# Kernel tuning notes

Hardware: AMD Instinct MI355X
Metric: run time of the kernel (lower is better)

The kernel has to match this reference:

```python
import jax, jax.numpy as jnp
import numpy as np

B_SZ, L, D_MODEL = 2, 1024, 1024
EXPAND, D_STATE, D_CONV = 2, 16, 4
D_INNER = D_MODEL * EXPAND
DT_RANK = max(D_MODEL // 16, 1)


def setup_inputs() -> dict:
    key = jax.random.key(0)
    ks = jax.random.split(key, 9)
    s = 0.02
    x = jax.random.normal(ks[0], (B_SZ, L, D_MODEL), jnp.float32)
    W_in = jax.random.normal(ks[1], (2 * D_INNER, D_MODEL), jnp.float32) * s
    conv_w = jax.random.normal(ks[2], (D_INNER, D_CONV), jnp.float32) * 0.1
    conv_b = jax.random.normal(ks[3], (D_INNER,), jnp.float32) * 0.01
    W_x = jax.random.normal(ks[4], (DT_RANK + 2 * D_STATE, D_INNER), jnp.float32) * s
    W_dt = jax.random.normal(ks[5], (D_INNER, DT_RANK), jnp.float32) * s
    b_dt = jax.random.normal(ks[6], (D_INNER,), jnp.float32) * 0.01
    A_log = jnp.log(jnp.broadcast_to(jnp.arange(1, D_STATE + 1, dtype=jnp.float32), (D_INNER, D_STATE)))
    D_param = jnp.ones((D_INNER,), jnp.float32)
    W_out = jax.random.normal(ks[7], (D_MODEL, D_INNER), jnp.float32) * s
    return {"x": x, "W_in": W_in, "conv_w": conv_w, "conv_b": conv_b,
            "W_x": W_x, "W_dt": W_dt, "b_dt": b_dt, "A_log": A_log,
            "D_param": D_param, "W_out": W_out}


def _mamba_fwd(x, W_in, conv_w, conv_b, W_x, W_dt, b_dt, A_log, D_param, W_out):
    # in-proj and gate split
    xz = jnp.einsum("bld,ed->ble", x, W_in)            # (B, L, 2*d_inner)
    x_ssm, z = jnp.split(xz, 2, axis=-1)
    # causal depthwise 1D conv (left pad d_conv-1 == torch pad-both + [:L])
    xc = x_ssm.transpose(0, 2, 1)                        # (B, d_inner, L)
    xc = jax.lax.conv_general_dilated(
        xc, conv_w[:, None, :], window_strides=(1,),
        padding=[(D_CONV - 1, 0)], feature_group_count=D_INNER,
        dimension_numbers=("NCH", "OIH", "NCH"))
    xc = xc + conv_b[None, :, None]
    x_ssm = jax.nn.silu(xc.transpose(0, 2, 1))           # (B, L, d_inner)
    # input-dependent dt, B, C
    dbc = jnp.einsum("bld,ed->ble", x_ssm, W_x)
    dt, B_sel, C_sel = jnp.split(dbc, [DT_RANK, DT_RANK + D_STATE], axis=-1)
    delta = jax.nn.softplus(jnp.einsum("blr,dr->bld", dt, W_dt) + b_dt)
    A = -jnp.exp(A_log)                                  # (d_inner, d_state)
    # discretization
    deltaA = jnp.exp(delta[..., None] * A)               # (B, L, d_inner, d_state)
    dBu = delta[..., None] * B_sel[:, :, None, :] * x_ssm[..., None]
    # linear recurrence h_t = deltaA_t * h_{t-1} + dBu_t via associative scan
    def comb(e1, e2):
        a1, b1 = e1
        a2, b2 = e2
        return (a1 * a2, a2 * b1 + b2)
    _, h = jax.lax.associative_scan(comb, (deltaA, dBu), axis=1)
    y = jnp.sum(h * C_sel[:, :, None, :], axis=-1)       # (B, L, d_inner)
    y = y + x_ssm * D_param
    y = y * jax.nn.silu(z)
    return jnp.einsum("ble,de->bld", y, W_out)


def reference(x, W_in, conv_w, conv_b, W_x, W_dt, b_dt, A_log, D_param, W_out):
    return _mamba_fwd(x, W_in, conv_w, conv_b, W_x, W_dt, b_dt, A_log, D_param, W_out)
```

## Files before the change

### kernel.cpp

```cpp
#include <hip/hip_runtime.h>
#include <hip/hip_bf16.h>

#define B_SZ   2
#define SEQ    1024
#define DMODEL 1024
#define DINNER 2048
#define DSTATE 16
#define DCONV  4
#define DTRANK 64
#define BLROWS (B_SZ*SEQ)
#define NCHUNK 32
#define TCHUNK (SEQ/NCHUNK)
#define NSLICE 16

using floatx4 = __attribute__((ext_vector_type(4))) float;
using short8  = __attribute__((ext_vector_type(8))) short;
using us8     = __attribute__((ext_vector_type(8))) unsigned short;
using us4     = __attribute__((ext_vector_type(4))) unsigned short;

__device__ __forceinline__ float softplus_f(float x) {
    return fmaxf(x, 0.f) + log1pf(__expf(-fabsf(x)));
}
__device__ __forceinline__ float silu_f(float x) {
    return x / (1.f + __expf(-x));
}
__device__ __forceinline__ short bfs(float x) {
    union { __hip_bfloat16 h; short s; } u;
    u.h = __float2bfloat16(x);
    return u.s;
}
__device__ __forceinline__ float b2f(unsigned short s) {
    union { float f; unsigned u; } x;
    x.u = ((unsigned)s) << 16;
    return x.f;
}
__device__ __forceinline__ void gld16(const void* g, void* l) {
    __builtin_amdgcn_global_load_lds((const __attribute__((address_space(1))) void*)g,
                                     (__attribute__((address_space(3))) void*)l,
                                     16, 0, 0);
}
__device__ __forceinline__ void cast8(const float* src, unsigned short* dst, int i) {
    const float* p = src + (size_t)i*8;
    float4 a = *(const float4*)p, b = *(const float4*)(p+4);
    us8 o;
    o[0]=(unsigned short)bfs(a.x); o[1]=(unsigned short)bfs(a.y);
    o[2]=(unsigned short)bfs(a.z); o[3]=(unsigned short)bfs(a.w);
    o[4]=(unsigned short)bfs(b.x); o[5]=(unsigned short)bfs(b.y);
    o[6]=(unsigned short)bfs(b.z); o[7]=(unsigned short)bfs(b.w);
    *(us8*)(dst + (size_t)i*8) = o;
}

#define G0 (BLROWS*DMODEL/8)
#define G1 (2*DINNER*DMODEL/8)
#define G2 (96*DINNER/8)
#define G3 (DINNER*DTRANK/8)
#define G4 (DMODEL*DINNER/8)
#define GTOT (G0+G1+G2+G3+G4)
__global__ __launch_bounds__(256)
void init_kernel(const float* __restrict__ x, const float* __restrict__ W_in,
                 const float* __restrict__ W_x, const float* __restrict__ W_dt,
                 const float* __restrict__ W_out,
                 unsigned short* xH, unsigned short* WinH, unsigned short* WxH,
                 unsigned short* WdtH, unsigned short* WoutH)
{
    int i = blockIdx.x*256 + threadIdx.x;
    if (i < G0) { cast8(x, xH, i); return; }            i -= G0;
    if (i < G1) { cast8(W_in, WinH, i); return; }       i -= G1;
    if (i < G2) { cast8(W_x, WxH, i); return; }         i -= G2;
    if (i < G3) { cast8(W_dt, WdtH, i); return; }       i -= G3;
    if (i < G4) { cast8(W_out, WoutH, i); }
}

template<int TN, int EPI, bool NGUARD>
__global__ __launch_bounds__(256)
void gemm_tn(const __hip_bfloat16* __restrict__ Ag, const __hip_bfloat16* __restrict__ Bg,
             int M, int N, int K, int kslice,
             float* __restrict__ outF,
             __hip_bfloat16* __restrict__ outH,
             __hip_bfloat16* __restrict__ outH2,
             const float* __restrict__ bias)
{
    constexpr int EB  = TN/64;
    constexpr int FNW = TN/32;
    __shared__ short As[2][128*32];
    __shared__ short Bs[2][TN*32];

    const int tid  = threadIdx.x;
    const int lane = tid & 63, wave = tid >> 6;
    const int bm0  = blockIdx.x * 128;
    const int bn0  = blockIdx.y * TN;
    const int kbeg = blockIdx.z * kslice;
    const int kend = kbeg + kslice;
    const int wrow = (wave >> 1) * 64, wcol = (wave & 1) * (TN/2);
    const int lrow = lane & 15, quad = lane >> 4;

    const int srow = wave*16 + (lane >> 2);
    const int scol = (lane & 3) * 8;

    const __hip_bfloat16* ga0 = Ag + (size_t)(bm0 + srow)*K      + scol;
    const __hip_bfloat16* ga1 = Ag + (size_t)(bm0 + srow + 64)*K + scol;
    const __hip_bfloat16* gb0 = Bg + (size_t)(bn0 + srow)*K      + scol;
    const __hip_bfloat16* gb1 = (EB > 1) ? Bg + (size_t)(bn0 + srow + 64)*K + scol : nullptr;
    const bool b0ok = !NGUARD || (bn0 + wave*16) < N;
    const bool b1ok = (EB > 1) && (!NGUARD || (bn0 + wave*16 + 64) < N);

    auto stage = [&](int c, int k0) {
        gld16(ga0 + k0, &As[c][(wave*16)*32]);
        gld16(ga1 + k0, &As[c][(wave*16 + 64)*32]);
        if (b0ok) gld16(gb0 + k0, &Bs[c][(wave*16)*32]);
        if (EB > 1 && b1ok) gld16(gb1 + k0, &Bs[c][(wave*16 + 64)*32]);
    };

    floatx4 acc[4][FNW] = {};

    stage(0, kbeg);
    __syncthreads();
    int cur = 0;
    for (int k0 = kbeg; k0 < kend; k0 += 32) {
        if (k0 + 32 < kend) stage(cur ^ 1, k0 + 32);
        short8 af[4], bf[FNW];
        #pragma unroll
        for (int i = 0; i < 4; i++)
            af[i] = *(const short8*)&As[cur][(wrow + i*16 + lrow)*32 + quad*8];
        #pragma unroll
        for (int j = 0; j < FNW; j++)
            bf[j] = *(const short8*)&Bs[cur][(wcol + j*16 + lrow)*32 + quad*8];
        #pragma unroll
        for (int i = 0; i < 4; i++)
            #pragma unroll
            for (int j = 0; j < FNW; j++)
                acc[i][j] = __builtin_amdgcn_mfma_f32_16x16x32_bf16(af[i], bf[j], acc[i][j], 0, 0, 0);
        __syncthreads();
        cur ^= 1;
    }

    const int rq = quad * 4;
    #pragma unroll
    for (int i = 0; i < 4; i++) {
        #pragma unroll
        for (int j = 0; j < FNW; j++) {
            int col = bn0 + wcol + j*16 + lrow;
            if (NGUARD && col >= N) continue;
            if constexpr (EPI == 8) {
                int row0 = bm0 + wrow + i*16 + rq;
                int bb = row0 >> 10, ll = row0 & (SEQ-1);
                us4 pk;
                #pragma unroll
                for (int r = 0; r < 4; r++)
                    pk[r] = (unsigned short)bfs(softplus_f(acc[i][j][r] + bias[col]));
                *(us4*)((unsigned short*)outH + ((size_t)bb*DINNER + col)*SEQ + ll) = pk;
            } else {
                #pragma unroll
                for (int r = 0; r < 4; r++) {
                    int row = bm0 + wrow + i*16 + rq + r;
                    float v = acc[i][j][r];
                    if constexpr (EPI == 5) {
                        if (col < DINNER)
                            outH[(size_t)row*DINNER + col] = __float2bfloat16(v);
                        else
                            outH2[(size_t)row*DINNER + (col - DINNER)] = __float2bfloat16(v);
                    } else if constexpr (EPI == 9) {
                        outF[(size_t)blockIdx.z*M*N + (size_t)row*N + col] = v;
                    }
                }
            }
        }
    }
}

__global__ __launch_bounds__(192)
void dbc_reduce_kernel(const float* __restrict__ part, float* __restrict__ dbc,
                       __hip_bfloat16* __restrict__ dtH)
{
    const int tid = threadIdx.x;
    const int r2  = (tid >= 96) ? 1 : 0;
    const int col = tid - 96*r2;
    const int row = blockIdx.x*2 + r2;
    const size_t idx = (size_t)row*96 + col;
    float s = 0.f;
    #pragma unroll
    for (int z = 0; z < NSLICE; z++)
        s += part[(size_t)z*(BLROWS*96) + idx];
    dbc[idx] = s;
    if (col < DTRANK)
        dtH[(size_t)row*DTRANK + col] = __float2bfloat16(s);
}

__global__ __launch_bounds__(256)
void conv_transpose_kernel(const unsigned short* __restrict__ xbufN,
                           const float* __restrict__ cw,
                           const float* __restrict__ cb,
                           unsigned short* __restrict__ xsN,
                           unsigned short* __restrict__ xsT)
{
    __shared__ unsigned short t[67*68];
    __shared__ unsigned short t2[64*68];
    const int tid = threadIdx.x;
    const int l0 = blockIdx.x * 64, d0 = blockIdx.y * 64, b = blockIdx.z;

    const int lc4 = (tid & 15) * 4;
    for (int r = tid >> 4; r < 67; r += 16) {
        int lg = l0 - 3 + r;
        us4 v = {0,0,0,0};
        if (lg >= 0)
            v = *(const us4*)&xbufN[((size_t)(b*SEQ + lg))*DINNER + d0 + lc4];
        *(us4*)&t[r*68 + lc4] = v;
    }
    __syncthreads();

    const int dd = tid & 63;
    float4 w4 = *(const float4*)&cw[(d0 + dd)*4];
    float  bb = cb[d0 + dd];
    #pragma unroll 4
    for (int rr = tid >> 6; rr < 64; rr += 4) {
        float acc = bb;
        acc += w4.x * b2f(t[(rr+0)*68 + dd]);
        acc += w4.y * b2f(t[(rr+1)*68 + dd]);
        acc += w4.z * b2f(t[(rr+2)*68 + dd]);
        acc += w4.w * b2f(t[(rr+3)*68 + dd]);
        unsigned short h = (unsigned short)bfs(silu_f(acc));
        t2[rr*68 + dd] = h;
        xsN[((size_t)(b*SEQ + l0 + rr))*DINNER + d0 + dd] = h;
    }
    __syncthreads();

    const int dr = tid >> 4, lc = tid & 15;
    #pragma unroll
    for (int i = 0; i < 4; i++) {
        int dT = dr + i*16;
        us4 w;
        #pragma unroll
        for (int j = 0; j < 4; j++)
            w[j] = t2[(lc*4 + j)*68 + dT];
        *(us4*)&xsT[((size_t)b*DINNER + d0 + dT)*SEQ + l0 + lc*4] = w;
    }
}

__global__ __launch_bounds__(256)
void scan_pass1(const unsigned short* __restrict__ deT,
                const unsigned short* __restrict__ xsT,
                const float* __restrict__ dbc,
                const float* __restrict__ A_log,
                float* __restrict__ Bc, float* __restrict__ sde)
{
    __shared__ float bs[TCHUNK*16];
    const int tid  = threadIdx.x;
    const int q    = tid & 3, dsub = tid >> 2;
    const int blk  = blockIdx.x;
    const int dg   = blk & 31;
    const int c    = (blk >> 5) & (NCHUNK-1);
    const int b    = blk >> 10;
    const int d    = dg*64 + dsub;

    size_t b96 = (size_t)b*SEQ*96;
    if (tid < TCHUNK*4) {
        int r = tid >> 2, f = (tid & 3) * 4;
        *(float4*)&bs[r*16 + f] =
            *(const float4*)&dbc[b96 + (size_t)(c*TCHUNK + r)*96 + DTRANK + f];
    }

    float An[4];
    *(float4*)An = *(const float4*)&A_log[d*DSTATE + 4*q];
    #pragma unroll
    for (int j = 0; j < 4; j++) An[j] = -__expf(An[j]);

    size_t rowT = ((size_t)b*DINNER + d)*SEQ;
    __syncthreads();

    float h[4] = {0.f,0.f,0.f,0.f};
    float s = 0.f;
    for (int t8 = 0; t8 < TCHUNK/8; ++t8) {
        int l0 = c*TCHUNK + t8*8;
        us8 de8 = *(const us8*)&deT[rowT + l0];
        us8 u8  = *(const us8*)&xsT[rowT + l0];
        #pragma unroll
        for (int j2 = 0; j2 < 8; j2++) {
            int lr = t8*8 + j2;
            float Bn[4];
            *(float4*)Bn = *(const float4*)&bs[lr*16 + 4*q];
            float de = b2f(de8[j2]);
            float du = de * b2f(u8[j2]);
            #pragma unroll
            for (int j = 0; j < 4; j++)
                h[j] = __expf(de*An[j])*h[j] + du*Bn[j];
            s += de;
        }
    }
    size_t ci = (size_t)(b*NCHUNK + c)*DINNER + d;
    *(float4*)&Bc[ci*16 + 4*q] = *(float4*)h;
    if (q == 0) sde[ci] = s;
}

__global__ __launch_bounds__(256)
void scan_pass2(float* __restrict__ Bc, const float* __restrict__ sde,
                const float* __restrict__ A_log)
{
    const int tid = threadIdx.x;
    const int n   = tid & 15, dl = tid >> 4;
    const int blk = blockIdx.x;
    const int dg  = blk & 127, b = blk >> 7;
    const int d   = dg*16 + dl;
    const float An = -__expf(A_log[d*DSTATE + n]);

    float H = 0.f;
    for (int c = 0; c < NCHUNK; ++c) {
        size_t ci = (size_t)(b*NCHUNK + c)*DINNER + d;
        float bc = Bc[ci*16 + n];
        Bc[ci*16 + n] = H;
        H = __expf(An*sde[ci])*H + bc;
    }
}

__global__ __launch_bounds__(256)
void scan_pass3(const unsigned short* __restrict__ deT,
                const unsigned short* __restrict__ xsT,
                const float* __restrict__ dbc,
                const float* __restrict__ A_log,
                const float* __restrict__ Dp,
                const float* __restrict__ Hinit,
                const unsigned short* __restrict__ zN,
                __hip_bfloat16* __restrict__ yN)
{
    __shared__ float bcs[TCHUNK*32];
    const int tid  = threadIdx.x;
    const int q    = tid & 3, dsub = tid >> 2;
    const int blk  = blockIdx.x;
    const int dg   = blk & 31;
    const int c    = (blk >> 5) & (NCHUNK-1);
    const int b    = blk >> 10;
    const int d    = dg*64 + dsub;

    size_t b96 = (size_t)b*SEQ*96;
    {
        int r = tid >> 3, f = (tid & 7) * 4;
        *(float4*)&bcs[r*32 + f] =
            *(const float4*)&dbc[b96 + (size_t)(c*TCHUNK + r)*96 + DTRANK + f];
    }

    float An[4];
    *(float4*)An = *(const float4*)&A_log[d*DSTATE + 4*q];
    #pragma unroll
    for (int j = 0; j < 4; j++) An[j] = -__expf(An[j]);
    const float Dd = Dp[d];

    size_t rowT  = ((size_t)b*DINNER + d)*SEQ;
    size_t baseN = (size_t)b*SEQ*DINNER + d;

    float h[4];
    *(float4*)h = *(const float4*)&Hinit[((size_t)(b*NCHUNK + c)*DINNER + d)*16 + 4*q];
    __syncthreads();

    for (int t8 = 0; t8 < TCHUNK/8; ++t8) {
        int l0 = c*TCHUNK + t8*8;
        us8 de8 = *(const us8*)&deT[rowT + l0];
        us8 u8  = *(const us8*)&xsT[rowT + l0];
        #pragma unroll
        for (int j2 = 0; j2 < 8; j2++) {
            int l  = l0 + j2;
            int lr = t8*8 + j2;
            float Bn[4], Cn[4];
            *(float4*)Bn = *(const float4*)&bcs[lr*32 + 4*q];
            *(float4*)Cn = *(const float4*)&bcs[lr*32 + 16 + 4*q];
            float de = b2f(de8[j2]);
            float u  = b2f(u8[j2]);
            float du = de * u;
            float cc = 0.f;
            #pragma unroll
            for (int j = 0; j < 4; j++) {
                h[j] = __expf(de*An[j])*h[j] + du*Bn[j];
                cc += h[j]*Cn[j];
            }
            cc += __shfl_xor(cc, 1);
            cc += __shfl_xor(cc, 2);
            if (q == 0) {
                float zv = silu_f(b2f(zN[baseN + (size_t)l*DINNER]));
                yN[baseN + (size_t)l*DINNER] = __float2bfloat16((cc + u*Dd) * zv);
            }
        }
    }
}

__global__ __launch_bounds__(256)
void zero_out_kernel(float* out, int n) {
    int i = blockIdx.x * 256 + threadIdx.x;
    if (i < n) out[i] = 0.f;
}

extern "C" void kernel_launch(void* const* d_in, const int* in_sizes, int n_in,
                              void* d_out, int out_size, void* d_ws, size_t ws_size,
                              hipStream_t stream) {
    const float* x      = (const float*)d_in[0];
    const float* W_in   = (const float*)d_in[1];
    const float* conv_w = (const float*)d_in[2];
    const float* conv_b = (const float*)d_in[3];
    const float* W_x    = (const float*)d_in[4];
    const float* W_dt   = (const float*)d_in[5];
    const float* b_dt   = (const float*)d_in[6];
    const float* A_log  = (const float*)d_in[7];
    const float* D_par  = (const float*)d_in[8];
    const float* W_out  = (const float*)d_in[9];

    size_t szBig = (size_t)BLROWS * DINNER * 2;
    size_t szBc  = (size_t)B_SZ * NCHUNK * DINNER * DSTATE * 4;
    size_t need  = 5*szBig
                 + (size_t)BLROWS*96*4
                 + (size_t)NSLICE*BLROWS*96*4
                 + (size_t)BLROWS*DTRANK*2
                 + szBc + (size_t)B_SZ*NCHUNK*DINNER*4
                 + (size_t)BLROWS*DMODEL*2
                 + (size_t)2*DINNER*DMODEL*2
                 + (size_t)128*DINNER*2
                 + (size_t)DINNER*DTRANK*2
                 + (size_t)DMODEL*DINNER*2;

    if (ws_size < need) {
        zero_out_kernel<<<(out_size + 255)/256, 256, 0, stream>>>((float*)d_out, out_size);
        return;
    }

    char* w = (char*)d_ws;
    __hip_bfloat16* xbufN = (__hip_bfloat16*)w;  w += szBig;
    __hip_bfloat16* zbufN = (__hip_bfloat16*)w;  w += szBig;
    __hip_bfloat16* xsN   = (__hip_bfloat16*)w;  w += szBig;
    __hip_bfloat16* xsT   = (__hip_bfloat16*)w;  w += szBig;
    __hip_bfloat16* deT   = (__hip_bfloat16*)w;  w += szBig;
    float*          dbc   = (float*)w;           w += (size_t)BLROWS * 96 * 4;
    float*          dbcP  = (float*)w;           w += (size_t)NSLICE * BLROWS * 96 * 4;
    __hip_bfloat16* dtH   = (__hip_bfloat16*)w;  w += (size_t)BLROWS * DTRANK * 2;
    float*          Bc    = (float*)w;           w += szBc;
    float*          sde   = (float*)w;           w += (size_t)B_SZ * NCHUNK * DINNER * 4;
    __hip_bfloat16* xH    = (__hip_bfloat16*)w;  w += (size_t)BLROWS*DMODEL*2;
    __hip_bfloat16* WinH  = (__hip_bfloat16*)w;  w += (size_t)2*DINNER*DMODEL*2;
    __hip_bfloat16* WxH   = (__hip_bfloat16*)w;  w += (size_t)128*DINNER*2;
    __hip_bfloat16* WdtH  = (__hip_bfloat16*)w;  w += (size_t)DINNER*DTRANK*2;
    __hip_bfloat16* WoutH = (__hip_bfloat16*)w;  w += (size_t)DMODEL*DINNER*2;
    __hip_bfloat16* yN    = xsN;

    init_kernel<<<GTOT/256, 256, 0, stream>>>(x, W_in, W_x, W_dt, W_out,
        (unsigned short*)xH, (unsigned short*)WinH, (unsigned short*)WxH,
        (unsigned short*)WdtH, (unsigned short*)WoutH);

    gemm_tn<128,5,false><<<dim3(BLROWS/128, (2*DINNER)/128, 1), 256, 0, stream>>>(
        xH, WinH, BLROWS, 2*DINNER, DMODEL, DMODEL, nullptr, xbufN, zbufN, nullptr);

    conv_transpose_kernel<<<dim3(SEQ/64, DINNER/64, B_SZ), 256, 0, stream>>>(
        (const unsigned short*)xbufN, conv_w, conv_b,
        (unsigned short*)xsN, (unsigned short*)xsT);

    gemm_tn<64,9,true><<<dim3(BLROWS/128, 2, NSLICE), 256, 0, stream>>>(
        xsN, WxH, BLROWS, 96, DINNER, DINNER/NSLICE, dbcP, nullptr, nullptr, nullptr);
    dbc_reduce_kernel<<<BLROWS/2, 192, 0, stream>>>(dbcP, dbc, dtH);

    gemm_tn<64,8,false><<<dim3(BLROWS/128, DINNER/64, 1), 256, 0, stream>>>(
        dtH, WdtH, BLROWS, DINNER, DTRANK, DTRANK, nullptr, deT, nullptr, b_dt);

    scan_pass1<<<B_SZ*NCHUNK*32, 256, 0, stream>>>((const unsigned short*)deT,
        (const unsigned short*)xsT, dbc, A_log, Bc, sde);
    scan_pass2<<<B_SZ*128, 256, 0, stream>>>(Bc, sde, A_log);
    scan_pass3<<<B_SZ*NCHUNK*32, 256, 0, stream>>>((const unsigned short*)deT,
        (const unsigned short*)xsT, dbc, A_log, D_par, Bc,
        (const unsigned short*)zbufN, yN);

    gemm_tn<64,9,false><<<dim3(BLROWS/128, DMODEL/64, 1), 256, 0, stream>>>(
        yN, WoutH, BLROWS, DMODEL, DINNER, DINNER, (float*)d_out, nullptr, nullptr, nullptr);
}
```

Measured before the change: 238.1 us.

## Split-K the output projection GEMM and use exp2 in the scan passes

```diff
diff --git a/kernel.cpp b/kernel.cpp
--- a/kernel.cpp
+++ b/kernel.cpp
@@ -12,6 +12,8 @@
 #define NCHUNK 32
 #define TCHUNK (SEQ/NCHUNK)
 #define NSLICE 16
+#define KSPLIT6 4
+#define LOG2E 1.44269504088896f
 
 using floatx4 = __attribute__((ext_vector_type(4))) float;
 using short8  = __attribute__((ext_vector_type(8))) short;
@@ -187,6 +189,19 @@
 }
 
 __global__ __launch_bounds__(256)
+void out_reduce_kernel(const float* __restrict__ part, float* __restrict__ out)
+{
+    size_t i = ((size_t)blockIdx.x*256 + threadIdx.x) * 4;
+    float4 s = *(const float4*)&part[i];
+    #pragma unroll
+    for (int z = 1; z < KSPLIT6; z++) {
+        float4 p = *(const float4*)&part[(size_t)z*((size_t)BLROWS*DMODEL) + i];
+        s.x += p.x; s.y += p.y; s.z += p.z; s.w += p.w;
+    }
+    *(float4*)&out[i] = s;
+}
+
+__global__ __launch_bounds__(256)
 void conv_transpose_kernel(const unsigned short* __restrict__ xbufN,
                            const float* __restrict__ cw,
                            const float* __restrict__ cb,
@@ -262,7 +277,7 @@
     float An[4];
     *(float4*)An = *(const float4*)&A_log[d*DSTATE + 4*q];
     #pragma unroll
-    for (int j = 0; j < 4; j++) An[j] = -__expf(An[j]);
+    for (int j = 0; j < 4; j++) An[j] = -__expf(An[j]) * LOG2E;
 
     size_t rowT = ((size_t)b*DINNER + d)*SEQ;
     __syncthreads();
@@ -282,7 +297,7 @@
             float du = de * b2f(u8[j2]);
             #pragma unroll
             for (int j = 0; j < 4; j++)
-                h[j] = __expf(de*An[j])*h[j] + du*Bn[j];
+                h[j] = exp2f(de*An[j])*h[j] + du*Bn[j];
             s += de;
         }
     }
@@ -300,14 +315,14 @@
     const int blk = blockIdx.x;
     const int dg  = blk & 127, b = blk >> 7;
     const int d   = dg*16 + dl;
-    const float An = -__expf(A_log[d*DSTATE + n]);
+    const float An = -__expf(A_log[d*DSTATE + n]) * LOG2E;
 
     float H = 0.f;
     for (int c = 0; c < NCHUNK; ++c) {
         size_t ci = (size_t)(b*NCHUNK + c)*DINNER + d;
         float bc = Bc[ci*16 + n];
         Bc[ci*16 + n] = H;
-        H = __expf(An*sde[ci])*H + bc;
+        H = exp2f(An*sde[ci])*H + bc;
     }
 }
 
@@ -340,7 +355,7 @@
     float An[4];
     *(float4*)An = *(const float4*)&A_log[d*DSTATE + 4*q];
     #pragma unroll
-    for (int j = 0; j < 4; j++) An[j] = -__expf(An[j]);
+    for (int j = 0; j < 4; j++) An[j] = -__expf(An[j]) * LOG2E;
     const float Dd = Dp[d];
 
     size_t rowT  = ((size_t)b*DINNER + d)*SEQ;
@@ -367,7 +382,7 @@
             float cc = 0.f;
             #pragma unroll
             for (int j = 0; j < 4; j++) {
-                h[j] = __expf(de*An[j])*h[j] + du*Bn[j];
+                h[j] = exp2f(de*An[j])*h[j] + du*Bn[j];
                 cc += h[j]*Cn[j];
             }
             cc += __shfl_xor(cc, 1);
@@ -402,11 +417,13 @@
 
     size_t szBig = (size_t)BLROWS * DINNER * 2;
     size_t szBc  = (size_t)B_SZ * NCHUNK * DINNER * DSTATE * 4;
+    size_t szP6  = (size_t)KSPLIT6 * BLROWS * DMODEL * 4;
     size_t need  = 5*szBig
                  + (size_t)BLROWS*96*4
                  + (size_t)NSLICE*BLROWS*96*4
                  + (size_t)BLROWS*DTRANK*2
                  + szBc + (size_t)B_SZ*NCHUNK*DINNER*4
+                 + szP6
                  + (size_t)BLROWS*DMODEL*2
                  + (size_t)2*DINNER*DMODEL*2
                  + (size_t)128*DINNER*2
@@ -429,6 +446,7 @@
     __hip_bfloat16* dtH   = (__hip_bfloat16*)w;  w += (size_t)BLROWS * DTRANK * 2;
     float*          Bc    = (float*)w;           w += szBc;
     float*          sde   = (float*)w;           w += (size_t)B_SZ * NCHUNK * DINNER * 4;
+    float*          outP6 = (float*)w;           w += szP6;
     __hip_bfloat16* xH    = (__hip_bfloat16*)w;  w += (size_t)BLROWS*DMODEL*2;
     __hip_bfloat16* WinH  = (__hip_bfloat16*)w;  w += (size_t)2*DINNER*DMODEL*2;
     __hip_bfloat16* WxH   = (__hip_bfloat16*)w;  w += (size_t)128*DINNER*2;
@@ -461,6 +479,7 @@
         (const unsigned short*)xsT, dbc, A_log, D_par, Bc,
         (const unsigned short*)zbufN, yN);
 
-    gemm_tn<64,9,false><<<dim3(BLROWS/128, DMODEL/64, 1), 256, 0, stream>>>(
-        yN, WoutH, BLROWS, DMODEL, DINNER, DINNER, (float*)d_out, nullptr, nullptr, nullptr);
-}
+    gemm_tn<64,9,false><<<dim3(BLROWS/128, DMODEL/64, KSPLIT6), 256, 0, stream>>>(
+        yN, WoutH, BLROWS, DMODEL, DINNER, DINNER/KSPLIT6, outP6, nullptr, nullptr, nullptr);
+    out_reduce_kernel<<<(BLROWS*DMODEL)/(256*4), 256, 0, stream>>>(outP6, (float*)d_out);
+}
```

Result: slower. 246.7 us (+3.6%).

## Compute local chunk outputs in pass1 and apply state correction in pass3

Applied to the files above, without the earlier changes.

```diff
diff --git a/kernel.cpp b/kernel.cpp
--- a/kernel.cpp
+++ b/kernel.cpp
@@ -12,6 +12,7 @@
 #define NCHUNK 32
 #define TCHUNK (SEQ/NCHUNK)
 #define NSLICE 16
+#define LOG2E 1.44269504088896f
 
 using floatx4 = __attribute__((ext_vector_type(4))) float;
 using short8  = __attribute__((ext_vector_type(8))) short;
@@ -236,90 +237,15 @@
     }
 }
 
+
 __global__ __launch_bounds__(256)
 void scan_pass1(const unsigned short* __restrict__ deT,
                 const unsigned short* __restrict__ xsT,
                 const float* __restrict__ dbc,
                 const float* __restrict__ A_log,
+                const float* __restrict__ Dp,
+                float* __restrict__ ylocF,
                 float* __restrict__ Bc, float* __restrict__ sde)
-{
-    __shared__ float bs[TCHUNK*16];
-    const int tid  = threadIdx.x;
-    const int q    = tid & 3, dsub = tid >> 2;
-    const int blk  = blockIdx.x;
-    const int dg   = blk & 31;
-    const int c    = (blk >> 5) & (NCHUNK-1);
-    const int b    = blk >> 10;
-    const int d    = dg*64 + dsub;
-
-    size_t b96 = (size_t)b*SEQ*96;
-    if (tid < TCHUNK*4) {
-        int r = tid >> 2, f = (tid & 3) * 4;
-        *(float4*)&bs[r*16 + f] =
-            *(const float4*)&dbc[b96 + (size_t)(c*TCHUNK + r)*96 + DTRANK + f];
-    }
-
-    float An[4];
-    *(float4*)An = *(const float4*)&A_log[d*DSTATE + 4*q];
-    #pragma unroll
-    for (int j = 0; j < 4; j++) An[j] = -__expf(An[j]);
-
-    size_t rowT = ((size_t)b*DINNER + d)*SEQ;
-    __syncthreads();
-
-    float h[4] = {0.f,0.f,0.f,0.f};
-    float s = 0.f;
-    for (int t8 = 0; t8 < TCHUNK/8; ++t8) {
-        int l0 = c*TCHUNK + t8*8;
-        us8 de8 = *(const us8*)&deT[rowT + l0];
-        us8 u8  = *(const us8*)&xsT[rowT + l0];
-        #pragma unroll
-        for (int j2 = 0; j2 < 8; j2++) {
-            int lr = t8*8 + j2;
-            float Bn[4];
-            *(float4*)Bn = *(const float4*)&bs[lr*16 + 4*q];
-            float de = b2f(de8[j2]);
-            float du = de * b2f(u8[j2]);
-            #pragma unroll
-            for (int j = 0; j < 4; j++)
-                h[j] = __expf(de*An[j])*h[j] + du*Bn[j];
-            s += de;
-        }
-    }
-    size_t ci = (size_t)(b*NCHUNK + c)*DINNER + d;
-    *(float4*)&Bc[ci*16 + 4*q] = *(float4*)h;
-    if (q == 0) sde[ci] = s;
-}
-
-__global__ __launch_bounds__(256)
-void scan_pass2(float* __restrict__ Bc, const float* __restrict__ sde,
-                const float* __restrict__ A_log)
-{
-    const int tid = threadIdx.x;
-    const int n   = tid & 15, dl = tid >> 4;
-    const int blk = blockIdx.x;
-    const int dg  = blk & 127, b = blk >> 7;
-    const int d   = dg*16 + dl;
-    const float An = -__expf(A_log[d*DSTATE + n]);
-
-    float H = 0.f;
-    for (int c = 0; c < NCHUNK; ++c) {
-        size_t ci = (size_t)(b*NCHUNK + c)*DINNER + d;
-        float bc = Bc[ci*16 + n];
-        Bc[ci*16 + n] = H;
-        H = __expf(An*sde[ci])*H + bc;
-    }
-}
-
-__global__ __launch_bounds__(256)
-void scan_pass3(const unsigned short* __restrict__ deT,
-                const unsigned short* __restrict__ xsT,
-                const float* __restrict__ dbc,
-                const float* __restrict__ A_log,
-                const float* __restrict__ Dp,
-                const float* __restrict__ Hinit,
-                const unsigned short* __restrict__ zN,
-                __hip_bfloat16* __restrict__ yN)
 {
     __shared__ float bcs[TCHUNK*32];
     const int tid  = threadIdx.x;
@@ -340,16 +266,15 @@
     float An[4];
     *(float4*)An = *(const float4*)&A_log[d*DSTATE + 4*q];
     #pragma unroll
-    for (int j = 0; j < 4; j++) An[j] = -__expf(An[j]);
+    for (int j = 0; j < 4; j++) An[j] = -__expf(An[j]) * LOG2E;
     const float Dd = Dp[d];
 
     size_t rowT  = ((size_t)b*DINNER + d)*SEQ;
     size_t baseN = (size_t)b*SEQ*DINNER + d;
-
-    float h[4];
-    *(float4*)h = *(const float4*)&Hinit[((size_t)(b*NCHUNK + c)*DINNER + d)*16 + 4*q];
     __syncthreads();
 
+    float h[4] = {0.f,0.f,0.f,0.f};
+    float s = 0.f;
     for (int t8 = 0; t8 < TCHUNK/8; ++t8) {
         int l0 = c*TCHUNK + t8*8;
         us8 de8 = *(const us8*)&deT[rowT + l0];
@@ -367,14 +292,99 @@
             float cc = 0.f;
             #pragma unroll
             for (int j = 0; j < 4; j++) {
-                h[j] = __expf(de*An[j])*h[j] + du*Bn[j];
+                h[j] = exp2f(de*An[j])*h[j] + du*Bn[j];
                 cc += h[j]*Cn[j];
             }
+            s += de;
             cc += __shfl_xor(cc, 1);
             cc += __shfl_xor(cc, 2);
+            if (q == 0)
+                ylocF[baseN + (size_t)l*DINNER] = cc + u*Dd;
+        }
+    }
+    size_t ci = (size_t)(b*NCHUNK + c)*DINNER + d;
+    *(float4*)&Bc[ci*16 + 4*q] = *(float4*)h;
+    if (q == 0) sde[ci] = s;
+}
+
+__global__ __launch_bounds__(256)
+void scan_pass2(float* __restrict__ Bc, const float* __restrict__ sde,
+                const float* __restrict__ A_log)
+{
+    const int tid = threadIdx.x;
+    const int n   = tid & 15, dl = tid >> 4;
+    const int blk = blockIdx.x;
+    const int dg  = blk & 127, b = blk >> 7;
+    const int d   = dg*16 + dl;
+    const float An = -__expf(A_log[d*DSTATE + n]) * LOG2E;
+
+    float H = 0.f;
+    for (int c = 0; c < NCHUNK; ++c) {
+        size_t ci = (size_t)(b*NCHUNK + c)*DINNER + d;
+        float bc = Bc[ci*16 + n];
+        Bc[ci*16 + n] = H;
+        H = exp2f(An*sde[ci])*H + bc;
+    }
+}
+
+__global__ __launch_bounds__(256)
+void scan_pass3(const unsigned short* __restrict__ deT,
+                const float* __restrict__ dbc,
+                const float* __restrict__ A_log,
+                const float* __restrict__ Hinit,
+                const float* __restrict__ ylocF,
+                const unsigned short* __restrict__ zN,
+                __hip_bfloat16* __restrict__ yN)
+{
+    __shared__ float cs[TCHUNK*16];
+    const int tid  = threadIdx.x;
+    const int q    = tid & 3, dsub = tid >> 2;
+    const int blk  = blockIdx.x;
+    const int dg   = blk & 31;
+    const int c    = (blk >> 5) & (NCHUNK-1);
+    const int b    = blk >> 10;
+    const int d    = dg*64 + dsub;
+
+    size_t b96 = (size_t)b*SEQ*96;
+    if (tid < TCHUNK*4) {
+        int r = tid >> 2, f = (tid & 3) * 4;
+        *(float4*)&cs[r*16 + f] =
+            *(const float4*)&dbc[b96 + (size_t)(c*TCHUNK + r)*96 + DTRANK + DSTATE + f];
+    }
+
+    float An[4];
+    *(float4*)An = *(const float4*)&A_log[d*DSTATE + 4*q];
+    #pragma unroll
+    for (int j = 0; j < 4; j++) An[j] = -__expf(An[j]) * LOG2E;
+
+    float H0[4];
+    *(float4*)H0 = *(const float4*)&Hinit[((size_t)(b*NCHUNK + c)*DINNER + d)*16 + 4*q];
+
+    size_t rowT  = ((size_t)b*DINNER + d)*SEQ;
+    size_t baseN = (size_t)b*SEQ*DINNER + d;
+    __syncthreads();
+
+    float s = 0.f;
+    for (int t8 = 0; t8 < TCHUNK/8; ++t8) {
+        int l0 = c*TCHUNK + t8*8;
+        us8 de8 = *(const us8*)&deT[rowT + l0];
+        #pragma unroll
+        for (int j2 = 0; j2 < 8; j2++) {
+            int l  = l0 + j2;
+            int lr = t8*8 + j2;
+            float Cn[4];
+            *(float4*)Cn = *(const float4*)&cs[lr*16 + 4*q];
+            s += b2f(de8[j2]);
+            float corr = 0.f;
+            #pragma unroll
+            for (int j = 0; j < 4; j++)
+                corr += Cn[j] * (exp2f(An[j]*s) * H0[j]);
+            corr += __shfl_xor(corr, 1);
+            corr += __shfl_xor(corr, 2);
             if (q == 0) {
+                float yl = ylocF[baseN + (size_t)l*DINNER];
                 float zv = silu_f(b2f(zN[baseN + (size_t)l*DINNER]));
-                yN[baseN + (size_t)l*DINNER] = __float2bfloat16((cc + u*Dd) * zv);
+                yN[baseN + (size_t)l*DINNER] = __float2bfloat16((yl + corr) * zv);
             }
         }
     }
@@ -402,11 +412,13 @@
 
     size_t szBig = (size_t)BLROWS * DINNER * 2;
     size_t szBc  = (size_t)B_SZ * NCHUNK * DINNER * DSTATE * 4;
+    size_t szYl  = (size_t)BLROWS * DINNER * 4;
     size_t need  = 5*szBig
                  + (size_t)BLROWS*96*4
                  + (size_t)NSLICE*BLROWS*96*4
                  + (size_t)BLROWS*DTRANK*2
                  + szBc + (size_t)B_SZ*NCHUNK*DINNER*4
+                 + szYl
                  + (size_t)BLROWS*DMODEL*2
                  + (size_t)2*DINNER*DMODEL*2
                  + (size_t)128*DINNER*2
@@ -429,6 +441,7 @@
     __hip_bfloat16* dtH   = (__hip_bfloat16*)w;  w += (size_t)BLROWS * DTRANK * 2;
     float*          Bc    = (float*)w;           w += szBc;
     float*          sde   = (float*)w;           w += (size_t)B_SZ * NCHUNK * DINNER * 4;
+    float*          ylocF = (float*)w;           w += szYl;
     __hip_bfloat16* xH    = (__hip_bfloat16*)w;  w += (size_t)BLROWS*DMODEL*2;
     __hip_bfloat16* WinH  = (__hip_bfloat16*)w;  w += (size_t)2*DINNER*DMODEL*2;
     __hip_bfloat16* WxH   = (__hip_bfloat16*)w;  w += (size_t)128*DINNER*2;
@@ -455,11 +468,10 @@
         dtH, WdtH, BLROWS, DINNER, DTRANK, DTRANK, nullptr, deT, nullptr, b_dt);
 
     scan_pass1<<<B_SZ*NCHUNK*32, 256, 0, stream>>>((const unsigned short*)deT,
-        (const unsigned short*)xsT, dbc, A_log, Bc, sde);
+        (const unsigned short*)xsT, dbc, A_log, D_par, ylocF, Bc, sde);
     scan_pass2<<<B_SZ*128, 256, 0, stream>>>(Bc, sde, A_log);
     scan_pass3<<<B_SZ*NCHUNK*32, 256, 0, stream>>>((const unsigned short*)deT,
-        (const unsigned short*)xsT, dbc, A_log, D_par, Bc,
-        (const unsigned short*)zbufN, yN);
+        dbc, A_log, Bc, ylocF, (const unsigned short*)zbufN, yN);
 
     gemm_tn<64,9,false><<<dim3(BLROWS/128, DMODEL/64, 1), 256, 0, stream>>>(
         yN, WoutH, BLROWS, DMODEL, DINNER, DINNER, (float*)d_out, nullptr, nullptr, nullptr);
```

Result: slower. 255.5 us (+7.3%).
